# Kernel tuning notes

Hardware: AMD Instinct MI355X
Metric: run time of the kernel (lower is better)

Reference implementation:

```python
import jax, jax.numpy as jnp
import numpy as np

M = 4        # num_modalities
C = 128      # in_channels
NH = 4       # num_heads
HD = C // NH # head_dim = 32
OUT = 128    # out_channels
B, D, H, W = 1, 12, 12, 12
N = D * H * W
EPS = 1e-5
SCALE = float(np.sqrt(HD))


def setup_inputs() -> dict:
    key = jax.random.key(0)
    ks = jax.random.split(key, 12)
    inp = {}
    for i in range(M):
        inp[f"feat{i}"] = jax.random.normal(ks[i], (B, C, D, H, W), dtype=jnp.float32)
    s = 1.0 / np.sqrt(C)
    inp["Wq"] = jax.random.normal(ks[4], (M, C, C), dtype=jnp.float32) * s
    inp["Wk"] = jax.random.normal(ks[5], (M, C, C), dtype=jnp.float32) * s
    inp["Wv"] = jax.random.normal(ks[6], (M, C, C), dtype=jnp.float32) * s
    inp["Wout"] = jax.random.normal(ks[7], (OUT, C), dtype=jnp.float32) * s
    inp["bn_gamma"] = jnp.ones((OUT,), jnp.float32)
    inp["bn_beta"] = jnp.zeros((OUT,), jnp.float32)
    inp["bn_mean"] = jax.random.normal(ks[8], (OUT,), dtype=jnp.float32) * 0.1
    inp["bn_var"] = jax.random.uniform(ks[9], (OUT,), dtype=jnp.float32, minval=0.5, maxval=1.5)
    return inp


def _proj(Wm, feats):
    # per-modality 1x1 conv == matmul over channels: [M,C,C] x [M,B,C,N] -> [M,B,nh,N,hd]
    p = jnp.einsum('moc,mbcn->mbon', Wm, feats)
    return p.reshape(M, B, NH, HD, N).transpose(0, 1, 2, 4, 3)


def reference(feat0, feat1, feat2, feat3, Wq, Wk, Wv, Wout,
              bn_gamma, bn_beta, bn_mean, bn_var):
    feats = jnp.stack([feat0, feat1, feat2, feat3]).reshape(M, B, C, N)
    Q = _proj(Wq, feats)   # [M,B,nh,N,hd]
    K = _proj(Wk, feats)
    V = _proj(Wv, feats)
    # concat K/V over modalities along token axis -> [B,nh,M*N,hd]
    Kall = K.transpose(1, 2, 0, 3, 4).reshape(B, NH, M * N, HD)
    Vall = V.transpose(1, 2, 0, 3, 4).reshape(B, NH, M * N, HD)
    fused = jnp.zeros((B, NH, N, HD), jnp.float32)
    for i in range(M):  # small fixed loop over modalities
        attn = jnp.einsum('bhqd,bhkd->bhqk', Q[i], Kall) / SCALE  # [B,nh,N,M*N]
        attn = jax.nn.softmax(attn, axis=-1)  # dropout is identity at eval
        fused = fused + jnp.einsum('bhqk,bhkd->bhqd', attn, Vall)
    fused = fused.transpose(0, 1, 3, 2).reshape(B, C, N)
    # out_proj: 1x1 Conv3d -> BN (eval, running stats) -> ReLU
    y = jnp.einsum('oc,bcn->bon', Wout, fused)
    inv = bn_gamma / jnp.sqrt(bn_var + EPS)
    y = y * inv[None, :, None] + (bn_beta - bn_mean * inv)[None, :, None]
    return jax.nn.relu(y).reshape(B, OUT, D, H, W)
```

## Files before the change

### kernel.cpp

```cpp
#include <hip/hip_runtime.h>

#define MODS 4
#define CH   128
#define NHD  4
#define HDIM 32
#define NTOK 1728
#define NKEY (MODS*NTOK)
#define NT   27
#define QSC (0.17677669529663687f * 1.4426950408889634f)

#ifndef __has_builtin
#define __has_builtin(x) 0
#endif
#if __has_builtin(__builtin_amdgcn_exp2f)
#define EXP2(x) __builtin_amdgcn_exp2f(x)
#else
#define EXP2(x) __expf(0.69314718055994531f * (x))
#endif

typedef __bf16 bf16x8 __attribute__((ext_vector_type(8)));
typedef float  f32x16 __attribute__((ext_vector_type(16)));

__device__ inline bf16x8 ldb8(const unsigned short* p) {
    return *reinterpret_cast<const bf16x8*>(p);
}
__device__ inline unsigned short bfc(float x) {
    return __builtin_bit_cast(unsigned short, (__bf16)x);
}
__device__ inline unsigned int pkbf(float a, float b) {
    return (unsigned int)bfc(a) | ((unsigned int)bfc(b) << 16);
}
__device__ inline void glds16(const unsigned short* g, unsigned short* l) {
    __builtin_amdgcn_global_load_lds(
        (const __attribute__((address_space(1))) unsigned int*)(g),
        (__attribute__((address_space(3))) unsigned int*)(l), 16, 0, 0);
}

__global__ __launch_bounds__(256) void prepw_kernel(
    const float* __restrict__ Wq, const float* __restrict__ Wk,
    const float* __restrict__ Wv, const float* __restrict__ Wout,
    unsigned short* __restrict__ Wb, unsigned short* __restrict__ WbO)
{
    const int gid = blockIdx.x * 256 + threadIdx.x;
    const size_t base = (size_t)gid * 16;
    const float* src; unsigned short* dst; float sc = 1.0f;
    if (base < 65536)       { src = Wq + base;            dst = Wb + base;  sc = QSC; }
    else if (base < 131072) { src = Wk + (base - 65536);  dst = Wb + base; }
    else if (base < 196608) { src = Wv + (base - 131072); dst = Wb + base; }
    else                    { src = Wout + (base - 196608); dst = WbO + (base - 196608); }
    #pragma unroll
    for (int g = 0; g < 4; ++g) {
        float4 v = *reinterpret_cast<const float4*>(src + g * 4);
        ushort4 pk;
        pk.x = bfc(v.x * sc); pk.y = bfc(v.y * sc);
        pk.z = bfc(v.z * sc); pk.w = bfc(v.w * sc);
        *reinterpret_cast<ushort4*>(dst + g * 4) = pk;
    }
}

__global__ __launch_bounds__(256) void proj_kernel(
    const float* __restrict__ f0, const float* __restrict__ f1,
    const float* __restrict__ f2, const float* __restrict__ f3,
    const unsigned short* __restrict__ Wb,
    unsigned short* __restrict__ Qb, unsigned short* __restrict__ Kb,
    unsigned short* __restrict__ V2)
{
    __shared__ __align__(16) unsigned short fT[32][136];
    __shared__ __align__(16) float accf[128 * 33];

    const int tid = threadIdx.x;
    const int lane = tid & 63;
    const int w    = tid >> 6;
    const int l31  = lane & 31;
    const int hi   = lane >> 5;

    const int bid = blockIdx.x;
    const int tm  = bid / 54;
    const int nb  = (bid % 54) * 32;
    const int t   = tm >> 2, m = tm & 3;

    const float* fsrc = (m == 0) ? f0 : (m == 1) ? f1 : (m == 2) ? f2 : f3;

    {
        const int n = tid & 31, cg = tid >> 5;
        float v[16];
        #pragma unroll
        for (int k = 0; k < 16; ++k)
            v[k] = fsrc[(size_t)(cg * 16 + k) * NTOK + nb + n];
        unsigned int* dst = reinterpret_cast<unsigned int*>(&fT[n][cg * 16]);
        #pragma unroll
        for (int j = 0; j < 8; ++j) dst[j] = pkbf(v[2 * j], v[2 * j + 1]);
    }
    __syncthreads();

    const unsigned short* Wrow = Wb + ((size_t)tm * CH + w * 32 + l31) * CH + hi * 8;
    f32x16 acc;
    #pragma unroll
    for (int r = 0; r < 16; ++r) acc[r] = 0.f;
    #pragma unroll
    for (int cc = 0; cc < 8; ++cc) {
        bf16x8 a = ldb8(Wrow + cc * 16);
        bf16x8 b = ldb8(&fT[l31][cc * 16 + hi * 8]);
        acc = __builtin_amdgcn_mfma_f32_32x32x16_bf16(a, b, acc, 0, 0, 0);
    }
    #pragma unroll
    for (int r = 0; r < 16; ++r) {
        const int orow = w * 32 + (r & 3) + 8 * (r >> 2) + 4 * hi;
        accf[orow * 33 + l31] = acc[r];
    }
    __syncthreads();

    if (t < 2) {
        unsigned short* dstb = (t == 0) ? Qb : Kb;
        const int nl = tid >> 3, dp = (tid & 7) * 4;
        #pragma unroll
        for (int h = 0; h < 4; ++h) {
            ushort4 pk;
            pk.x = bfc(accf[(h * 32 + dp + 0) * 33 + nl]);
            pk.y = bfc(accf[(h * 32 + dp + 1) * 33 + nl]);
            pk.z = bfc(accf[(h * 32 + dp + 2) * 33 + nl]);
            pk.w = bfc(accf[(h * 32 + dp + 3) * 33 + nl]);
            *reinterpret_cast<ushort4*>(
                dstb + (((size_t)(m * NHD + h)) * NTOK + nb + nl) * HDIM + dp) = pk;
        }
    } else {
        const int row = tid >> 1, half = tid & 1;
        const int nw = half * 16;
        unsigned short* dst = V2 + (size_t)row * NKEY + (size_t)m * NTOK + nb + nw;
        const float* src = &accf[row * 33 + nw];
        ushort4 p0, p1, p2, p3;
        p0.x = bfc(src[0]);  p0.y = bfc(src[1]);  p0.z = bfc(src[2]);  p0.w = bfc(src[3]);
        p1.x = bfc(src[8]);  p1.y = bfc(src[9]);  p1.z = bfc(src[10]); p1.w = bfc(src[11]);
        p2.x = bfc(src[4]);  p2.y = bfc(src[5]);  p2.z = bfc(src[6]);  p2.w = bfc(src[7]);
        p3.x = bfc(src[12]); p3.y = bfc(src[13]); p3.z = bfc(src[14]); p3.w = bfc(src[15]);
        *reinterpret_cast<ushort4*>(dst + 0)  = p0;
        *reinterpret_cast<ushort4*>(dst + 4)  = p1;
        *reinterpret_cast<ushort4*>(dst + 8)  = p2;
        *reinterpret_cast<ushort4*>(dst + 12) = p3;
    }
}

__global__ __launch_bounds__(256, 6) void attn_kernel(
    const unsigned short* __restrict__ Qb, const unsigned short* __restrict__ Kb,
    const unsigned short* __restrict__ V2,
    float* __restrict__ accT, float* __restrict__ sR)
{
    __shared__ __align__(16) unsigned short smAll[2][2][2][1024];

    const int tid  = threadIdx.x;
    const int lane = tid & 63;
    const int w    = tid >> 6;
    const int qslot = w & 1;
    const int ks    = w >> 1;
    const int l31  = lane & 31;
    const int hi   = lane >> 5;

    const int bid  = blockIdx.x;
    const int slot = bid & 7;
    const int h    = slot >> 1;
    const int ko   = slot & 1;
    const int rest = bid >> 3;
    const int qb   = rest % 108;
    const int kseg = rest / 108;
    const int qtile = qb * 2 + qslot;
    const int qg0  = qtile * 32;
    const int im   = qg0 / NTOK;
    const int n0   = qg0 % NTOK;
    const int km   = ko * 2 + ks;
    const int p    = kseg * 2 + ko;

    const unsigned short* qp = Qb + (((size_t)(im * NHD + h)) * NTOK + n0 + l31) * HDIM + hi * 8;
    const bf16x8 qf0 = ldb8(qp);
    const bf16x8 qf1 = ldb8(qp + 16);

    const int rk0 = qslot * 16 + (lane >> 2);
    const int ck0 = (lane & 3) ^ ((rk0 >> 1) & 3);
    const unsigned short* gk0 = Kb
        + (((size_t)(km * NHD + h)) * NTOK + kseg * 864 + rk0) * HDIM + ck0 * 8;
    const int dv0 = qslot * 16 + (lane >> 2);
    const int cv0 = (lane & 3) ^ (dv0 & 3);
    const unsigned short* gv0 = V2
        + ((size_t)(h * HDIM + dv0)) * NKEY + km * NTOK + kseg * 864 + cv0 * 8;

    const int fK = (l31 >> 1) & 3, fV = l31 & 3;
    const int kA0 = l31 * 32 + ((hi ^ fK) << 3);
    const int kB0 = l31 * 32 + (((2 + hi) ^ fK) << 3);
    const int vo0 = l31 * 32 + ((hi ^ fV) << 3);
    const int vo1 = l31 * 32 + (((2 + hi) ^ fV) << 3);

    f32x16 z;
    #pragma unroll
    for (int r = 0; r < 16; ++r) z[r] = 0.f;
    f32x16 o_acc = z, s_acc = z;
    bf16x8 onesv;
    #pragma unroll
    for (int j = 0; j < 8; ++j) onesv[j] = (__bf16)1.0f;

    #define STAGE(bb) do {                                      \
        glds16(gk0, &smAll[bb][ks][0][0] + qslot * 512);        \
        glds16(gv0, &smAll[bb][ks][1][0] + qslot * 512);        \
        gk0 += 1024; gv0 += 32;                                 \
    } while (0)

    STAGE(0);
    __syncthreads();

    int buf = 0;
    for (int t = 0; t < NT; ++t) {
        if (t + 1 < NT) STAGE(buf ^ 1);
        const unsigned short* Kl = &smAll[buf][ks][0][0];
        const unsigned short* Vl = &smAll[buf][ks][1][0];

        bf16x8 k0 = ldb8(Kl + kA0);
        bf16x8 k1 = ldb8(Kl + kB0);
        f32x16 c = __builtin_amdgcn_mfma_f32_32x32x16_bf16(k0, qf0, z, 0, 0, 0);
        c = __builtin_amdgcn_mfma_f32_32x32x16_bf16(k1, qf1, c, 0, 0, 0);

        float e[16];
        #pragma unroll
        for (int r = 0; r < 16; ++r) e[r] = EXP2(c[r]);
        bf16x8 pa0, pa1;
        #pragma unroll
        for (int j = 0; j < 8; ++j) { pa0[j] = (__bf16)e[j]; pa1[j] = (__bf16)e[8 + j]; }

        bf16x8 v0 = ldb8(Vl + vo0);
        bf16x8 v1 = ldb8(Vl + vo1);

        o_acc = __builtin_amdgcn_mfma_f32_32x32x16_bf16(pa0, v0, o_acc, 0, 0, 0);
        o_acc = __builtin_amdgcn_mfma_f32_32x32x16_bf16(pa1, v1, o_acc, 0, 0, 0);
        s_acc = __builtin_amdgcn_mfma_f32_32x32x16_bf16(pa0, onesv, s_acc, 0, 0, 0);
        s_acc = __builtin_amdgcn_mfma_f32_32x32x16_bf16(pa1, onesv, s_acc, 0, 0, 0);

        __syncthreads();
        buf ^= 1;
    }
    #undef STAGE

    float* accfL = (float*)&smAll[0][0][0][0];
    if (ks == 1) {
        #pragma unroll
        for (int r = 0; r < 16; ++r) {
            const int qrow = (r & 3) + 8 * (r >> 2) + 4 * hi;
            accfL[(qslot * 32 + qrow) * 33 + l31] = o_acc[r];
            if (l31 == 0) accfL[(qslot * 32 + qrow) * 33 + 32] = s_acc[r];
        }
    }
    __syncthreads();
    if (ks == 0) {
        #pragma unroll
        for (int r = 0; r < 16; ++r) {
            const int qrow = (r & 3) + 8 * (r >> 2) + 4 * hi;
            accfL[(qslot * 32 + qrow) * 33 + l31] += o_acc[r];
            if (l31 == 0) accfL[(qslot * 32 + qrow) * 33 + 32] += s_acc[r];
        }
    }
    __syncthreads();
    {
        const int q  = tid & 63;
        const int dq = tid >> 6;
        #pragma unroll
        for (int j = 0; j < 8; ++j) {
            const int d = dq * 8 + j;
            accT[((size_t)((p * 4 + h) * HDIM + d)) * NKEY + (size_t)qb * 64 + q]
                = accfL[q * 33 + d];
        }
        if (tid < 64)
            sR[((size_t)(p * 4 + h)) * NKEY + (size_t)qb * 64 + tid] = accfL[tid * 33 + 32];
    }
}

__global__ __launch_bounds__(256) void normout_kernel(
    const float* __restrict__ accT, const float* __restrict__ sR,
    const unsigned short* __restrict__ WbO,
    const float* __restrict__ gamma, const float* __restrict__ beta,
    const float* __restrict__ mean,  const float* __restrict__ var,
    float* __restrict__ out)
{
    __shared__ __align__(16) unsigned short fT2[32][136];
    __shared__ float rsL[4][4][32];

    const int tid = threadIdx.x;
    const int nb  = blockIdx.x * 32;

    #pragma unroll
    for (int e2 = 0; e2 < 2; ++e2) {
        const int e = tid * 2 + e2;
        const int h = e >> 7, imq = (e >> 5) & 3, n = e & 31;
        float s = 0.f;
        #pragma unroll
        for (int pp = 0; pp < 4; ++pp)
            s += sR[(size_t)(pp * 4 + h) * NKEY + (size_t)imq * NTOK + nb + n];
        rsL[h][imq][n] = 1.0f / s;
    }
    __syncthreads();

    {
        const int n4 = (tid & 7) * 4;
        const int c0 = (tid >> 3) * 4;
        const int h  = c0 >> 5;
        float acc4[4][4] = {};
        #pragma unroll
        for (int imq = 0; imq < 4; ++imq) {
            const size_t q = (size_t)imq * NTOK + nb + n4;
            float a[4][4] = {};
            #pragma unroll
            for (int pp = 0; pp < 4; ++pp) {
                #pragma unroll
                for (int cc = 0; cc < 4; ++cc) {
                    const int d = (c0 + cc) & 31;
                    float4 x = *reinterpret_cast<const float4*>(
                        accT + ((size_t)((pp * 4 + h) * HDIM + d)) * NKEY + q);
                    a[cc][0] += x.x; a[cc][1] += x.y; a[cc][2] += x.z; a[cc][3] += x.w;
                }
            }
            #pragma unroll
            for (int cc = 0; cc < 4; ++cc)
                #pragma unroll
                for (int nn = 0; nn < 4; ++nn)
                    acc4[cc][nn] = fmaf(a[cc][nn], rsL[h][imq][n4 + nn], acc4[cc][nn]);
        }
        #pragma unroll
        for (int nn = 0; nn < 4; ++nn) {
            ushort4 pk;
            pk.x = bfc(acc4[0][nn]); pk.y = bfc(acc4[1][nn]);
            pk.z = bfc(acc4[2][nn]); pk.w = bfc(acc4[3][nn]);
            *reinterpret_cast<ushort4*>(&fT2[n4 + nn][c0]) = pk;
        }
    }
    __syncthreads();

    {
        const int lane = tid & 63;
        const int w    = tid >> 6;
        const int l31  = lane & 31;
        const int hi   = lane >> 5;
        const unsigned short* Arow = WbO + (size_t)(w * 32 + l31) * CH + hi * 8;
        f32x16 acc;
        #pragma unroll
        for (int r = 0; r < 16; ++r) acc[r] = 0.f;
        #pragma unroll
        for (int cc = 0; cc < 8; ++cc) {
            bf16x8 a = ldb8(Arow + cc * 16);
            bf16x8 b = ldb8(&fT2[l31][cc * 16 + hi * 8]);
            acc = __builtin_amdgcn_mfma_f32_32x32x16_bf16(a, b, acc, 0, 0, 0);
        }
        #pragma unroll
        for (int r = 0; r < 16; ++r) {
            const int orow = w * 32 + (r & 3) + 8 * (r >> 2) + 4 * hi;
            const float inv = gamma[orow] * rsqrtf(var[orow] + 1e-5f);
            const float sh  = fmaf(-mean[orow], inv, beta[orow]);
            out[(size_t)orow * NTOK + nb + l31] = fmaxf(fmaf(acc[r], inv, sh), 0.f);
        }
    }
}

extern "C" void kernel_launch(void* const* d_in, const int* in_sizes, int n_in,
                              void* d_out, int out_size, void* d_ws, size_t ws_size,
                              hipStream_t stream)
{
    const float* f0    = (const float*)d_in[0];
    const float* f1    = (const float*)d_in[1];
    const float* f2    = (const float*)d_in[2];
    const float* f3    = (const float*)d_in[3];
    const float* Wq    = (const float*)d_in[4];
    const float* Wk    = (const float*)d_in[5];
    const float* Wv    = (const float*)d_in[6];
    const float* Wout  = (const float*)d_in[7];
    const float* gamma = (const float*)d_in[8];
    const float* beta  = (const float*)d_in[9];
    const float* mean  = (const float*)d_in[10];
    const float* var   = (const float*)d_in[11];
    float* out = (float*)d_out;

    const size_t QKV = (size_t)MODS * NHD * NTOK * HDIM;
    unsigned short* Qb  = (unsigned short*)d_ws;
    unsigned short* Kb  = Qb + QKV;
    unsigned short* V2  = Kb + QKV;
    unsigned short* Wb  = V2 + QKV;
    unsigned short* WbO = Wb + 196608;
    float* accT = (float*)(WbO + 16384);
    float* sR   = accT + (size_t)512 * NKEY;

    prepw_kernel<<<52, 256, 0, stream>>>(Wq, Wk, Wv, Wout, Wb, WbO);
    proj_kernel<<<648, 256, 0, stream>>>(f0, f1, f2, f3, Wb, Qb, Kb, V2);
    attn_kernel<<<1728, 256, 0, stream>>>(Qb, Kb, V2, accT, sR);
    normout_kernel<<<54, 256, 0, stream>>>(
        accT, sR, WbO, gamma, beta, mean, var, out);
}
```

Baseline: 70.81 us.

## Fold weight bf16 conversion into proj/normout kernels and widen normout blocks

Removes the separate weight-prep kernel launch. The fp32 weights are now converted to bf16 (with the Q scale applied) inside the projection and output kernels, right where they are loaded. The normout kernel also moves to 512 threads per block, each handling 2 channels instead of 4, to add parallelism to the reduction over accT. The trade-off is that each proj block now reads fp32 weights (twice the bytes) and converts them redundantly, in exchange for one fewer launch and less serialization.

```diff
diff --git a/kernel.cpp b/kernel.cpp
--- a/kernel.cpp
+++ b/kernel.cpp
@@ -20,6 +20,7 @@
 
 typedef __bf16 bf16x8 __attribute__((ext_vector_type(8)));
 typedef float  f32x16 __attribute__((ext_vector_type(16)));
+typedef unsigned int u32x4 __attribute__((ext_vector_type(4)));
 
 __device__ inline bf16x8 ldb8(const unsigned short* p) {
     return *reinterpret_cast<const bf16x8*>(p);
@@ -29,6 +30,13 @@
 }
 __device__ inline unsigned int pkbf(float a, float b) {
     return (unsigned int)bfc(a) | ((unsigned int)bfc(b) << 16);
+}
+__device__ inline bf16x8 cvt8(const float* p, float sc) {
+    float4 x = *reinterpret_cast<const float4*>(p);
+    float4 y = *reinterpret_cast<const float4*>(p + 4);
+    u32x4 u = {pkbf(x.x * sc, x.y * sc), pkbf(x.z * sc, x.w * sc),
+               pkbf(y.x * sc, y.y * sc), pkbf(y.z * sc, y.w * sc)};
+    return __builtin_bit_cast(bf16x8, u);
 }
 __device__ inline void glds16(const unsigned short* g, unsigned short* l) {
     __builtin_amdgcn_global_load_lds(
@@ -36,32 +44,11 @@
         (__attribute__((address_space(3))) unsigned int*)(l), 16, 0, 0);
 }
 
-__global__ __launch_bounds__(256) void prepw_kernel(
-    const float* __restrict__ Wq, const float* __restrict__ Wk,
-    const float* __restrict__ Wv, const float* __restrict__ Wout,
-    unsigned short* __restrict__ Wb, unsigned short* __restrict__ WbO)
-{
-    const int gid = blockIdx.x * 256 + threadIdx.x;
-    const size_t base = (size_t)gid * 16;
-    const float* src; unsigned short* dst; float sc = 1.0f;
-    if (base < 65536)       { src = Wq + base;            dst = Wb + base;  sc = QSC; }
-    else if (base < 131072) { src = Wk + (base - 65536);  dst = Wb + base; }
-    else if (base < 196608) { src = Wv + (base - 131072); dst = Wb + base; }
-    else                    { src = Wout + (base - 196608); dst = WbO + (base - 196608); }
-    #pragma unroll
-    for (int g = 0; g < 4; ++g) {
-        float4 v = *reinterpret_cast<const float4*>(src + g * 4);
-        ushort4 pk;
-        pk.x = bfc(v.x * sc); pk.y = bfc(v.y * sc);
-        pk.z = bfc(v.z * sc); pk.w = bfc(v.w * sc);
-        *reinterpret_cast<ushort4*>(dst + g * 4) = pk;
-    }
-}
-
 __global__ __launch_bounds__(256) void proj_kernel(
     const float* __restrict__ f0, const float* __restrict__ f1,
     const float* __restrict__ f2, const float* __restrict__ f3,
-    const unsigned short* __restrict__ Wb,
+    const float* __restrict__ Wq, const float* __restrict__ Wk,
+    const float* __restrict__ Wv,
     unsigned short* __restrict__ Qb, unsigned short* __restrict__ Kb,
     unsigned short* __restrict__ V2)
 {
@@ -80,6 +67,8 @@
     const int t   = tm >> 2, m = tm & 3;
 
     const float* fsrc = (m == 0) ? f0 : (m == 1) ? f1 : (m == 2) ? f2 : f3;
+    const float* Wsrc = ((t == 0) ? Wq : (t == 1) ? Wk : Wv) + (size_t)m * CH * CH;
+    const float  wsc  = (t == 0) ? QSC : 1.0f;
 
     {
         const int n = tid & 31, cg = tid >> 5;
@@ -93,13 +82,13 @@
     }
     __syncthreads();
 
-    const unsigned short* Wrow = Wb + ((size_t)tm * CH + w * 32 + l31) * CH + hi * 8;
+    const float* Wrow = Wsrc + (size_t)(w * 32 + l31) * CH + hi * 8;
     f32x16 acc;
     #pragma unroll
     for (int r = 0; r < 16; ++r) acc[r] = 0.f;
     #pragma unroll
     for (int cc = 0; cc < 8; ++cc) {
-        bf16x8 a = ldb8(Wrow + cc * 16);
+        bf16x8 a = cvt8(Wrow + cc * 16, wsc);
         bf16x8 b = ldb8(&fT[l31][cc * 16 + hi * 8]);
         acc = __builtin_amdgcn_mfma_f32_32x32x16_bf16(a, b, acc, 0, 0, 0);
     }
@@ -269,9 +258,9 @@
     }
 }
 
-__global__ __launch_bounds__(256) void normout_kernel(
+__global__ __launch_bounds__(512) void normout_kernel(
     const float* __restrict__ accT, const float* __restrict__ sR,
-    const unsigned short* __restrict__ WbO,
+    const float* __restrict__ Wout,
     const float* __restrict__ gamma, const float* __restrict__ beta,
     const float* __restrict__ mean,  const float* __restrict__ var,
     float* __restrict__ out)
@@ -282,10 +271,8 @@
     const int tid = threadIdx.x;
     const int nb  = blockIdx.x * 32;
 
-    #pragma unroll
-    for (int e2 = 0; e2 < 2; ++e2) {
-        const int e = tid * 2 + e2;
-        const int h = e >> 7, imq = (e >> 5) & 3, n = e & 31;
+    {
+        const int h = tid >> 7, imq = (tid >> 5) & 3, n = tid & 31;
         float s = 0.f;
         #pragma unroll
         for (int pp = 0; pp < 4; ++pp)
@@ -296,17 +283,17 @@
 
     {
         const int n4 = (tid & 7) * 4;
-        const int c0 = (tid >> 3) * 4;
+        const int c0 = (tid >> 3) * 2;
         const int h  = c0 >> 5;
-        float acc4[4][4] = {};
+        float acc4[2][4] = {};
         #pragma unroll
         for (int imq = 0; imq < 4; ++imq) {
             const size_t q = (size_t)imq * NTOK + nb + n4;
-            float a[4][4] = {};
+            float a[2][4] = {};
             #pragma unroll
             for (int pp = 0; pp < 4; ++pp) {
                 #pragma unroll
-                for (int cc = 0; cc < 4; ++cc) {
+                for (int cc = 0; cc < 2; ++cc) {
                     const int d = (c0 + cc) & 31;
                     float4 x = *reinterpret_cast<const float4*>(
                         accT + ((size_t)((pp * 4 + h) * HDIM + d)) * NKEY + q);
@@ -314,33 +301,32 @@
                 }
             }
             #pragma unroll
-            for (int cc = 0; cc < 4; ++cc)
+            for (int cc = 0; cc < 2; ++cc)
                 #pragma unroll
                 for (int nn = 0; nn < 4; ++nn)
                     acc4[cc][nn] = fmaf(a[cc][nn], rsL[h][imq][n4 + nn], acc4[cc][nn]);
         }
         #pragma unroll
         for (int nn = 0; nn < 4; ++nn) {
-            ushort4 pk;
+            ushort2 pk;
             pk.x = bfc(acc4[0][nn]); pk.y = bfc(acc4[1][nn]);
-            pk.z = bfc(acc4[2][nn]); pk.w = bfc(acc4[3][nn]);
-            *reinterpret_cast<ushort4*>(&fT2[n4 + nn][c0]) = pk;
-        }
-    }
-    __syncthreads();
-
-    {
+            *reinterpret_cast<ushort2*>(&fT2[n4 + nn][c0]) = pk;
+        }
+    }
+    __syncthreads();
+
+    if (tid < 256) {
         const int lane = tid & 63;
         const int w    = tid >> 6;
         const int l31  = lane & 31;
         const int hi   = lane >> 5;
-        const unsigned short* Arow = WbO + (size_t)(w * 32 + l31) * CH + hi * 8;
+        const float* Arow = Wout + (size_t)(w * 32 + l31) * CH + hi * 8;
         f32x16 acc;
         #pragma unroll
         for (int r = 0; r < 16; ++r) acc[r] = 0.f;
         #pragma unroll
         for (int cc = 0; cc < 8; ++cc) {
-            bf16x8 a = ldb8(Arow + cc * 16);
+            bf16x8 a = cvt8(Arow + cc * 16, 1.0f);
             bf16x8 b = ldb8(&fT2[l31][cc * 16 + hi * 8]);
             acc = __builtin_amdgcn_mfma_f32_32x32x16_bf16(a, b, acc, 0, 0, 0);
         }
@@ -376,14 +362,11 @@
     unsigned short* Qb  = (unsigned short*)d_ws;
     unsigned short* Kb  = Qb + QKV;
     unsigned short* V2  = Kb + QKV;
-    unsigned short* Wb  = V2 + QKV;
-    unsigned short* WbO = Wb + 196608;
-    float* accT = (float*)(WbO + 16384);
+    float* accT = (float*)(V2 + QKV);
     float* sR   = accT + (size_t)512 * NKEY;
 
-    prepw_kernel<<<52, 256, 0, stream>>>(Wq, Wk, Wv, Wout, Wb, WbO);
-    proj_kernel<<<648, 256, 0, stream>>>(f0, f1, f2, f3, Wb, Qb, Kb, V2);
+    proj_kernel<<<648, 256, 0, stream>>>(f0, f1, f2, f3, Wq, Wk, Wv, Qb, Kb, V2);
     attn_kernel<<<1728, 256, 0, stream>>>(Qb, Kb, V2, accT, sR);
-    normout_kernel<<<54, 256, 0, stream>>>(
-        accT, sR, WbO, gamma, beta, mean, var, out);
-}
+    normout_kernel<<<54, 512, 0, stream>>>(
+        accT, sR, Wout, gamma, beta, mean, var, out);
+}
```

New measurement: 65.89 us (median of 2 runs). 7.0% less time.
